# Performance work log

Hardware: AMD Instinct MI355X
Metric: run time of the kernel (lower is better)

## Reference

```python
import jax, jax.numpy as jnp
import numpy as np

N_OBSERVED = 64
N_LATENT = 64
N_NODES = N_OBSERVED + N_LATENT
M = 2                # max parents per node (BA attachment param)
N_SAMPLES = 262144
CAL_N = 256
CAL_FRAC = 0.1
SIGMA_W = 1.0


def _build_dag():
    """BA-style DAG in topological order: node i picks min(M, i) earlier parents."""
    rng = np.random.default_rng(0)
    par_idx = np.zeros((N_NODES, M), np.int32)
    par_mask = np.zeros((N_NODES, M), np.float32)
    is_root = np.zeros(N_NODES, bool)
    for i in range(N_NODES):
        k = min(M, i)
        if k == 0:
            is_root[i] = True
            continue
        ps = rng.choice(i, size=k, replace=False)
        par_idx[i, :k] = ps
        par_mask[i, :k] = 1.0
    has_child = np.zeros(N_NODES, bool)
    for i in range(N_NODES):
        for j in range(M):
            if par_mask[i, j] > 0:
                has_child[par_idx[i, j]] = True
    leaves = np.where(~has_child)[0]
    pool = leaves if len(leaves) >= N_OBSERVED else np.arange(N_NODES)
    chosen = rng.choice(pool, size=N_OBSERVED, replace=False).astype(np.int32)
    return par_idx, par_mask, is_root, chosen


def setup_inputs() -> dict:
    par_idx, par_mask, is_root, chosen = _build_dag()
    wrng = np.random.default_rng(1)
    n_par = par_mask.sum(axis=1)
    std = SIGMA_W / np.sqrt(np.maximum(n_par, 1.0))  # nn.init.normal_(std=sigma_w/sqrt(n_parents))
    W = (wrng.standard_normal((N_NODES, M)) * std[:, None] * par_mask).astype(np.float32)
    b = np.zeros(N_NODES, np.float32)                # bias zero-initialised
    key = jax.random.key(0)
    k1, k2, k3 = jax.random.split(key, 3)
    return {
        "n_samples": N_SAMPLES,
        "W": jnp.asarray(W),
        "b": jnp.asarray(b),
        "root_pilot": jax.random.normal(k1, (N_NODES, CAL_N), jnp.float32),
        "root_main": jax.random.normal(k2, (N_NODES, N_SAMPLES), jnp.float32),
        "z_noise": jax.random.normal(k3, (N_NODES, N_SAMPLES), jnp.float32),
        "par_mask": jnp.asarray(par_mask),
        "par_idx": jnp.asarray(par_idx),
        "is_root": jnp.asarray(is_root),
        "chosen": jnp.asarray(chosen),
    }


def _run_dag(W, b, par_mask, par_idx, is_root, roots, noise):
    """Topological scan: x_i = relu(w_i . x_parents + b_i) + noise_i, roots ~ given."""
    n = roots.shape[1]

    def step(vals, inp):
        i, pidx, pmask, w, bb, root_v, nz, rt = inp
        pv = vals[pidx]                                   # [M, n] gather parents
        h = jax.nn.relu(jnp.einsum("p,pn->n", w * pmask, pv) + bb) + nz
        v = jnp.where(rt, root_v, h)
        v = jnp.where(jnp.isfinite(v), v, jnp.zeros_like(v))
        vals = jax.lax.dynamic_update_slice(vals, v[None, :], (i, 0))
        return vals, None

    vals0 = jnp.zeros((N_NODES, n), roots.dtype)
    xs = (jnp.arange(N_NODES), par_idx, par_mask, W, b, roots, noise, is_root)
    vals, _ = jax.lax.scan(step, vals0, xs)
    return vals


def reference(n_samples, W, b, root_pilot, root_main, z_noise, par_mask, par_idx, is_root, chosen):
    # noise calibration: noiseless pilot pass, sigma_e = frac * IQR per node
    pilot = _run_dag(W, b, par_mask, par_idx, is_root, root_pilot, jnp.zeros_like(root_pilot))
    q75 = jnp.quantile(pilot, 0.75, axis=1)
    q25 = jnp.quantile(pilot, 0.25, axis=1)
    sigma_e = CAL_FRAC * jnp.maximum(q75 - q25, 1e-6)     # [N_NODES]
    # main pass with calibrated per-node noise
    vals = _run_dag(W, b, par_mask, par_idx, is_root, root_main, z_noise * sigma_e[:, None])
    return vals[chosen].T                                  # [n_samples, n_observed]
```

## Files before the change

kernel.cpp:

```cpp
#include <hip/hip_runtime.h>
#include <hip/hip_fp16.h>
#include <math.h>

#define NN   128
#define BS   64
#define SCAP 1056
#define RT_F 0x10000

#define IDX(n,t) ((n)*BS + ((t) ^ (((n)&15)<<1)))


__global__ __launch_bounds__(256) void prep_pilot_kernel(
    const float* __restrict__ W, const float* __restrict__ b,
    const float* __restrict__ pm, const int* __restrict__ pidx,
    const float* __restrict__ root_pilot,
    float4* __restrict__ wtab, int* __restrict__ pcode,
    int* __restrict__ slotmap, int* __restrict__ ngp,
    float* __restrict__ pilot_out, int CAL)
{
    __shared__ _Float16 vals[NN * 256];
    __shared__ int grp[NN], slot[NN], wcnt[4];
    __shared__ int nassigned, gdone, gfin;
    const int i = threadIdx.x, w = i >> 6, lane = i & 63;

    int p0 = 0, p1 = 0, rt = 1;
    float m0 = 0.f, m1 = 0.f;
    if (i < NN) {
        m0 = pm[2*i]; m1 = pm[2*i+1];
        p0 = pidx[2*i]; p1 = pidx[2*i+1];
        rt = (m0 == 0.0f && m1 == 0.0f) ? 1 : 0;
        grp[i] = -1; slot[i] = 0;
    }
    if (i == 0) { nassigned = 0; gdone = 0; gfin = 0; }
    __syncthreads();
    for (int g = 0; g < NN; ++g) {
        int ready = (i < NN) && (grp[i] < 0) && (rt || (grp[p0] >= 0 && grp[p1] >= 0));
        unsigned long long mask = __ballot(ready);
        if (lane == 0) wcnt[w] = __popcll(mask);
        __syncthreads();
        int base = 0;
        #pragma unroll
        for (int ww = 0; ww < 4; ++ww) if (ww < w) base += wcnt[ww];
        int r = base + __popcll(mask & ((1ull << lane) - 1ull));
        if (ready && r < 8) { grp[i] = g; slot[i] = g*8 + r; }
        if (i == 0) {
            int tot = wcnt[0] + wcnt[1] + wcnt[2] + wcnt[3];
            nassigned += min(tot, 8);
            if (nassigned >= NN) { gdone = 1; gfin = g; }
        }
        __syncthreads();
        if (gdone) break;
    }
    const int S0 = 8 * (gfin + 1);
    const int S  = (S0 + 31) & ~31;
    for (int k = i; k < SCAP; k += 256) {
        pcode[k] = RT_F;
        wtab[k]  = make_float4(0.f, 0.f, 0.f, 0.f);
    }
    __threadfence_block();
    __syncthreads();
    if (i < NN) {
        pcode[slot[i]] = p0 | (p1 << 8) | (rt << 16) | (i << 24);
        wtab[slot[i]]  = make_float4(W[2*i]*m0, W[2*i+1]*m1, b[i], 0.f);
        slotmap[i] = slot[i];
    }
    if (i == 0) ngp[0] = S;
    __threadfence_block();
    __syncthreads();

    const int jj = i;
    for (int s0 = 0; s0 < S; s0 += 8) {
        int pc[8]; float4 wv[8];
        #pragma unroll
        for (int u = 0; u < 8; ++u) pc[u] = pcode[s0 + u];
        #pragma unroll
        for (int u = 0; u < 8; ++u) wv[u] = wtab[s0 + u];
        float pa[8], pb[8];
        #pragma unroll
        for (int u = 0; u < 8; ++u) {
            int q0 = pc[u] & 0xff, q1 = (pc[u] >> 8) & 0xff;
            pa[u] = (float)vals[q0 * 256 + jj];
            pb[u] = (float)vals[q1 * 256 + jj];
        }
        _Float16 res[8]; int nodes[8]; float vf[8];
        #pragma unroll
        for (int u = 0; u < 8; ++u) {
            nodes[u] = (pc[u] >> 24) & 0xff;
            float v;
            if (pc[u] & RT_F) {
                v = root_pilot[nodes[u] * CAL + jj];
            } else {
                v = fmaxf(fmaf(wv[u].x, pa[u], fmaf(wv[u].y, pb[u], wv[u].z)), 0.0f);
            }
            if (!isfinite(v)) v = 0.0f;
            vf[u] = v; res[u] = (_Float16)v;
        }
        #pragma unroll
        for (int u = 0; u < 8; ++u) {
            vals[nodes[u] * 256 + jj] = res[u];
            pilot_out[nodes[u] * CAL + jj] = vf[u];
        }
    }
}

__global__ __launch_bounds__(256) void quant_kernel(
    const float* __restrict__ pilot, const int* __restrict__ slotmap,
    float4* __restrict__ wtab, int CAL)
{
    __shared__ float s[256];
    const int tid = threadIdx.x;
    const int node = blockIdx.x;
    s[tid] = pilot[(size_t)node * CAL + tid];
    __syncthreads();
    for (int k = 2; k <= 256; k <<= 1) {
        for (int jj = k >> 1; jj > 0; jj >>= 1) {
            int ixj = tid ^ jj;
            if (ixj > tid) {
                float a = s[tid], bv = s[ixj];
                bool up = ((tid & k) == 0);
                if ((a > bv) == up) { s[tid] = bv; s[ixj] = a; }
            }
            __syncthreads();
        }
    }
    if (tid == 0) {
        float q25 = s[63]  + 0.75f * (s[64]  - s[63]);
        float q75 = s[191] + 0.25f * (s[192] - s[191]);
        ((float*)&wtab[slotmap[node]])[3] = 0.1f * fmaxf(q75 - q25, 1e-6f);
    }
}

__device__ __forceinline__ void mk_chunk(
    int c, int P, float (&zb)[2][16],
    const int* __restrict__ pcode, const float4* __restrict__ wtab,
    const float* __restrict__ root_main, const float* __restrict__ z,
    unsigned NS, size_t j, _Float16* vals, int tid)
{
    const int base = c * 16;
    #pragma unroll
    for (int u = 0; u < 16; ++u) {
        int pcN = pcode[base + 16 + u];
        const float* src = (pcN & RT_F) ? root_main : z;
        unsigned node = (unsigned)(pcN >> 24) & 0xffu;
        zb[P ^ 1][u] = src[(size_t)(node * NS) + j];
    }
    #pragma unroll
    for (int h = 0; h < 2; ++h) {
        int pc[8];
        #pragma unroll
        for (int u = 0; u < 8; ++u) pc[u] = pcode[base + h*8 + u];
        float pa[8], pb[8];
        #pragma unroll
        for (int u = 0; u < 8; ++u) {
            int q0 = pc[u] & 0xff, q1 = (pc[u] >> 8) & 0xff;
            pa[u] = (float)vals[IDX(q0, tid)];
            pb[u] = (float)vals[IDX(q1, tid)];
        }
        _Float16 res[8]; int nodes[8];
        #pragma unroll
        for (int u = 0; u < 8; ++u) {
            float4 wv = wtab[base + h*8 + u];
            float zv = zb[P][h*8 + u];
            float v;
            if (pc[u] & RT_F) {
                v = zv;
            } else {
                v = fmaxf(fmaf(wv.x, pa[u], fmaf(wv.y, pb[u], wv.z)), 0.0f) + wv.w * zv;
            }
            if (!isfinite(v)) v = 0.0f;
            nodes[u] = (pc[u] >> 24) & 0xff;
            res[u] = (_Float16)v;
        }
        #pragma unroll
        for (int u = 0; u < 8; ++u) vals[IDX(nodes[u], tid)] = res[u];
    }
}

__global__ __launch_bounds__(64) void main_kernel(
    const float4* __restrict__ wtab, const int* __restrict__ pcode,
    const int* __restrict__ ngp,
    const float* __restrict__ root_main, const float* __restrict__ z,
    const int* __restrict__ chosen, float* __restrict__ out, int NSi)
{
    __shared__ _Float16 vals[NN * BS];
    const int tid = threadIdx.x;
    const size_t j = (size_t)blockIdx.x * BS + tid;
    const unsigned NS = (unsigned)NSi;
    const int S = ngp[0];
    const int nch = S >> 4;

    float zb[2][16];
    #pragma unroll
    for (int u = 0; u < 16; ++u) {
        int pc = pcode[u];
        const float* src = (pc & RT_F) ? root_main : z;
        unsigned node = (unsigned)(pc >> 24) & 0xffu;
        zb[0][u] = src[(size_t)(node * NS) + j];
    }

    for (int c = 0; c < nch; c += 2) {
        mk_chunk(c,     0, zb, pcode, wtab, root_main, z, NS, j, vals, tid);
        mk_chunk(c + 1, 1, zb, pcode, wtab, root_main, z, NS, j, vals, tid);
    }

    __syncthreads();

    float4* out4 = (float4*)(out + (size_t)blockIdx.x * BS * 64);
    #pragma unroll
    for (int it = 0; it < 16; ++it) {
        int cc = it * BS + tid;
        int s  = cc >> 4;
        int k0 = (cc & 15) << 2;
        int n0 = chosen[k0], n1 = chosen[k0+1], n2 = chosen[k0+2], n3 = chosen[k0+3];
        float4 o;
        o.x = (float)vals[IDX(n0, s)];
        o.y = (float)vals[IDX(n1, s)];
        o.z = (float)vals[IDX(n2, s)];
        o.w = (float)vals[IDX(n3, s)];
        out4[cc] = o;
    }
}

extern "C" void kernel_launch(void* const* d_in, const int* in_sizes, int n_in,
                              void* d_out, int out_size, void* d_ws, size_t ws_size,
                              hipStream_t stream) {
    const float* W          = (const float*)d_in[1];
    const float* b          = (const float*)d_in[2];
    const float* root_pilot = (const float*)d_in[3];
    const float* root_main  = (const float*)d_in[4];
    const float* z          = (const float*)d_in[5];
    const float* pm         = (const float*)d_in[6];
    const int*   pidx       = (const int*)d_in[7];
    const int*   chosen     = (const int*)d_in[9];
    float* out = (float*)d_out;

    const int NS  = in_sizes[4] / NN;
    const int CAL = in_sizes[3] / NN;

    char* ws = (char*)d_ws;
    float4* wtab    = (float4*)ws;
    int*    pcode   = (int*)(ws + 20480);
    int*    slotmap = (int*)(ws + 24704);
    int*    ngp     = (int*)(ws + 25216);
    float*  pilot   = (float*)(ws + 28672);

    prep_pilot_kernel<<<1, 256, 0, stream>>>(W, b, pm, pidx, root_pilot,
                                             wtab, pcode, slotmap, ngp, pilot, CAL);
    quant_kernel<<<NN, 256, 0, stream>>>(pilot, slotmap, wtab, CAL);
    main_kernel <<<NS / BS, BS, 0, stream>>>(wtab, pcode, ngp, root_main, z, chosen, out, NS);
}
```

Baseline: 337.9 us.

## Process two samples per thread with packed half2 shared storage and skip padding slots

Each thread in the main kernel now handles two adjacent samples, loading root/noise values as float2 and storing both results packed as a 32-bit half pair in shared memory with a new XOR swizzle. Padding slots in the schedule get a skip flag, so no global loads, shared reads or writes are issued for them in either the pilot or main kernel. This halves the grid size and the per-sample instruction overhead, at the cost of more registers per thread and fewer waves to hide memory latency.

```diff
diff --git a/kernel.cpp b/kernel.cpp
--- a/kernel.cpp
+++ b/kernel.cpp
@@ -2,12 +2,13 @@
 #include <hip/hip_fp16.h>
 #include <math.h>
 
-#define NN   128
-#define BS   64
-#define SCAP 1056
-#define RT_F 0x10000
-
-#define IDX(n,t) ((n)*BS + ((t) ^ (((n)&15)<<1)))
+#define NN    128
+#define SPB   128
+#define SCAP  1056
+#define RT_F  0x10000
+#define SK_F  0x20000
+
+#define WIDX(n,t) ((n)*64 + ((t) ^ ((n)&31)))
 
 
 __global__ __launch_bounds__(256) void prep_pilot_kernel(
@@ -54,7 +55,7 @@
     const int S0 = 8 * (gfin + 1);
     const int S  = (S0 + 31) & ~31;
     for (int k = i; k < SCAP; k += 256) {
-        pcode[k] = RT_F;
+        pcode[k] = RT_F | SK_F;
         wtab[k]  = make_float4(0.f, 0.f, 0.f, 0.f);
     }
     __threadfence_block();
@@ -78,27 +79,26 @@
         float pa[8], pb[8];
         #pragma unroll
         for (int u = 0; u < 8; ++u) {
-            int q0 = pc[u] & 0xff, q1 = (pc[u] >> 8) & 0xff;
-            pa[u] = (float)vals[q0 * 256 + jj];
-            pb[u] = (float)vals[q1 * 256 + jj];
-        }
-        _Float16 res[8]; int nodes[8]; float vf[8];
-        #pragma unroll
-        for (int u = 0; u < 8; ++u) {
-            nodes[u] = (pc[u] >> 24) & 0xff;
+            pa[u] = 0.f; pb[u] = 0.f;
+            if (!(pc[u] & (SK_F | RT_F))) {
+                int q0 = pc[u] & 0xff, q1 = (pc[u] >> 8) & 0xff;
+                pa[u] = (float)vals[q0 * 256 + jj];
+                pb[u] = (float)vals[q1 * 256 + jj];
+            }
+        }
+        #pragma unroll
+        for (int u = 0; u < 8; ++u) {
+            if (pc[u] & SK_F) continue;
+            int node = (pc[u] >> 24) & 0xff;
             float v;
             if (pc[u] & RT_F) {
-                v = root_pilot[nodes[u] * CAL + jj];
+                v = root_pilot[node * CAL + jj];
             } else {
                 v = fmaxf(fmaf(wv[u].x, pa[u], fmaf(wv[u].y, pb[u], wv[u].z)), 0.0f);
             }
             if (!isfinite(v)) v = 0.0f;
-            vf[u] = v; res[u] = (_Float16)v;
-        }
-        #pragma unroll
-        for (int u = 0; u < 8; ++u) {
-            vals[nodes[u] * 256 + jj] = res[u];
-            pilot_out[nodes[u] * CAL + jj] = vf[u];
+            vals[node * 256 + jj] = (_Float16)v;
+            pilot_out[node * CAL + jj] = v;
         }
     }
 }
@@ -131,48 +131,62 @@
 }
 
 __device__ __forceinline__ void mk_chunk(
-    int c, int P, float (&zb)[2][16],
+    int c, int P, float2 (&zb)[2][16],
     const int* __restrict__ pcode, const float4* __restrict__ wtab,
     const float* __restrict__ root_main, const float* __restrict__ z,
-    unsigned NS, size_t j, _Float16* vals, int tid)
+    unsigned NS, size_t j2, unsigned* vals, int tid)
 {
     const int base = c * 16;
     #pragma unroll
     for (int u = 0; u < 16; ++u) {
         int pcN = pcode[base + 16 + u];
-        const float* src = (pcN & RT_F) ? root_main : z;
-        unsigned node = (unsigned)(pcN >> 24) & 0xffu;
-        zb[P ^ 1][u] = src[(size_t)(node * NS) + j];
+        if (!(pcN & SK_F)) {
+            const float* src = (pcN & RT_F) ? root_main : z;
+            unsigned node = (unsigned)(pcN >> 24) & 0xffu;
+            zb[P ^ 1][u] = *(const float2*)(src + (size_t)node * NS + j2);
+        }
     }
     #pragma unroll
     for (int h = 0; h < 2; ++h) {
         int pc[8];
         #pragma unroll
         for (int u = 0; u < 8; ++u) pc[u] = pcode[base + h*8 + u];
-        float pa[8], pb[8];
-        #pragma unroll
-        for (int u = 0; u < 8; ++u) {
-            int q0 = pc[u] & 0xff, q1 = (pc[u] >> 8) & 0xff;
-            pa[u] = (float)vals[IDX(q0, tid)];
-            pb[u] = (float)vals[IDX(q1, tid)];
-        }
-        _Float16 res[8]; int nodes[8];
-        #pragma unroll
-        for (int u = 0; u < 8; ++u) {
+        unsigned wa[8], wb[8];
+        #pragma unroll
+        for (int u = 0; u < 8; ++u) {
+            wa[u] = 0u; wb[u] = 0u;
+            if (!(pc[u] & (SK_F | RT_F))) {
+                int q0 = pc[u] & 0xff, q1 = (pc[u] >> 8) & 0xff;
+                wa[u] = vals[WIDX(q0, tid)];
+                wb[u] = vals[WIDX(q1, tid)];
+            }
+        }
+        unsigned res[8]; int nodes[8];
+        #pragma unroll
+        for (int u = 0; u < 8; ++u) {
+            nodes[u] = (pc[u] >> 24) & 0xff;
             float4 wv = wtab[base + h*8 + u];
-            float zv = zb[P][h*8 + u];
-            float v;
+            float2 zv = zb[P][h*8 + u];
+            float v0, v1;
             if (pc[u] & RT_F) {
-                v = zv;
+                v0 = zv.x; v1 = zv.y;
             } else {
-                v = fmaxf(fmaf(wv.x, pa[u], fmaf(wv.y, pb[u], wv.z)), 0.0f) + wv.w * zv;
-            }
-            if (!isfinite(v)) v = 0.0f;
-            nodes[u] = (pc[u] >> 24) & 0xff;
-            res[u] = (_Float16)v;
-        }
-        #pragma unroll
-        for (int u = 0; u < 8; ++u) vals[IDX(nodes[u], tid)] = res[u];
+                union { unsigned u32; _Float16 h2[2]; } ua, ub;
+                ua.u32 = wa[u]; ub.u32 = wb[u];
+                float a0 = (float)ua.h2[0], a1 = (float)ua.h2[1];
+                float b0 = (float)ub.h2[0], b1 = (float)ub.h2[1];
+                v0 = fmaxf(fmaf(wv.x, a0, fmaf(wv.y, b0, wv.z)), 0.0f) + wv.w * zv.x;
+                v1 = fmaxf(fmaf(wv.x, a1, fmaf(wv.y, b1, wv.z)), 0.0f) + wv.w * zv.y;
+            }
+            if (!isfinite(v0)) v0 = 0.0f;
+            if (!isfinite(v1)) v1 = 0.0f;
+            union { unsigned u32; _Float16 h2[2]; } up;
+            up.h2[0] = (_Float16)v0; up.h2[1] = (_Float16)v1;
+            res[u] = up.u32;
+        }
+        #pragma unroll
+        for (int u = 0; u < 8; ++u)
+            if (!(pc[u] & SK_F)) vals[WIDX(nodes[u], tid)] = res[u];
     }
 }
 
@@ -182,41 +196,49 @@
     const float* __restrict__ root_main, const float* __restrict__ z,
     const int* __restrict__ chosen, float* __restrict__ out, int NSi)
 {
-    __shared__ _Float16 vals[NN * BS];
+    __shared__ unsigned vals[NN * 64];
     const int tid = threadIdx.x;
-    const size_t j = (size_t)blockIdx.x * BS + tid;
+    const size_t j2 = (size_t)blockIdx.x * SPB + (size_t)(tid * 2);
     const unsigned NS = (unsigned)NSi;
     const int S = ngp[0];
     const int nch = S >> 4;
 
-    float zb[2][16];
+    float2 zb[2][16];
     #pragma unroll
     for (int u = 0; u < 16; ++u) {
         int pc = pcode[u];
-        const float* src = (pc & RT_F) ? root_main : z;
-        unsigned node = (unsigned)(pc >> 24) & 0xffu;
-        zb[0][u] = src[(size_t)(node * NS) + j];
+        if (!(pc & SK_F)) {
+            const float* src = (pc & RT_F) ? root_main : z;
+            unsigned node = (unsigned)(pc >> 24) & 0xffu;
+            zb[0][u] = *(const float2*)(src + (size_t)node * NS + j2);
+        }
     }
 
     for (int c = 0; c < nch; c += 2) {
-        mk_chunk(c,     0, zb, pcode, wtab, root_main, z, NS, j, vals, tid);
-        mk_chunk(c + 1, 1, zb, pcode, wtab, root_main, z, NS, j, vals, tid);
-    }
-
-    __syncthreads();
-
-    float4* out4 = (float4*)(out + (size_t)blockIdx.x * BS * 64);
-    #pragma unroll
-    for (int it = 0; it < 16; ++it) {
-        int cc = it * BS + tid;
+        mk_chunk(c,     0, zb, pcode, wtab, root_main, z, NS, j2, vals, tid);
+        mk_chunk(c + 1, 1, zb, pcode, wtab, root_main, z, NS, j2, vals, tid);
+    }
+
+    __syncthreads();
+
+    float4* out4 = (float4*)(out + (size_t)blockIdx.x * SPB * 64);
+    #pragma unroll
+    for (int it = 0; it < 32; ++it) {
+        int cc = it * 64 + tid;
         int s  = cc >> 4;
         int k0 = (cc & 15) << 2;
         int n0 = chosen[k0], n1 = chosen[k0+1], n2 = chosen[k0+2], n3 = chosen[k0+3];
+        int tt = s >> 1, hh = s & 1;
+        union { unsigned u32; _Float16 h2[2]; } c0, c1, c2, c3;
+        c0.u32 = vals[WIDX(n0, tt)];
+        c1.u32 = vals[WIDX(n1, tt)];
+        c2.u32 = vals[WIDX(n2, tt)];
+        c3.u32 = vals[WIDX(n3, tt)];
         float4 o;
-        o.x = (float)vals[IDX(n0, s)];
-        o.y = (float)vals[IDX(n1, s)];
-        o.z = (float)vals[IDX(n2, s)];
-        o.w = (float)vals[IDX(n3, s)];
+        o.x = (float)c0.h2[hh];
+        o.y = (float)c1.h2[hh];
+        o.z = (float)c2.h2[hh];
+        o.w = (float)c3.h2[hh];
         out4[cc] = o;
     }
 }
@@ -247,5 +269,5 @@
     prep_pilot_kernel<<<1, 256, 0, stream>>>(W, b, pm, pidx, root_pilot,
                                              wtab, pcode, slotmap, ngp, pilot, CAL);
     quant_kernel<<<NN, 256, 0, stream>>>(pilot, slotmap, wtab, CAL);
-    main_kernel <<<NS / BS, BS, 0, stream>>>(wtab, pcode, ngp, root_main, z, chosen, out, NS);
-}
+    main_kernel <<<NS / SPB, 64, 0, stream>>>(wtab, pcode, ngp, root_main, z, chosen, out, NS);
+}
```

New measurement: 361.4 us. 1.07x slower.

## Deepen noise prefetch to four chunks and skip padding slots in DAG evaluation

Applied to the files above, without the earlier changes.

The main kernel now keeps four 16-slot chunks of root/noise loads in flight instead of a double buffer, which hides more global-memory latency behind the serial DAG computation. Padding slots get a skip flag, so they issue no global loads, no LDS reads and no stores. The slot count is rounded up to a multiple of 64 and the workspace offsets are widened to fit. The change raises register pressure (64 prefetch floats per thread) and adds per-slot branches.

```diff
diff --git a/kernel.cpp b/kernel.cpp
--- a/kernel.cpp
+++ b/kernel.cpp
@@ -2,10 +2,11 @@
 #include <hip/hip_fp16.h>
 #include <math.h>
 
-#define NN   128
-#define BS   64
-#define SCAP 1056
-#define RT_F 0x10000
+#define NN    128
+#define BS    64
+#define SCAP  1280
+#define RT_F  0x10000
+#define SK_F  0x20000
 
 #define IDX(n,t) ((n)*BS + ((t) ^ (((n)&15)<<1)))
 
@@ -52,9 +53,9 @@
         if (gdone) break;
     }
     const int S0 = 8 * (gfin + 1);
-    const int S  = (S0 + 31) & ~31;
+    const int S  = (S0 + 63) & ~63;
     for (int k = i; k < SCAP; k += 256) {
-        pcode[k] = RT_F;
+        pcode[k] = RT_F | SK_F;
         wtab[k]  = make_float4(0.f, 0.f, 0.f, 0.f);
     }
     __threadfence_block();
@@ -78,27 +79,26 @@
         float pa[8], pb[8];
         #pragma unroll
         for (int u = 0; u < 8; ++u) {
-            int q0 = pc[u] & 0xff, q1 = (pc[u] >> 8) & 0xff;
-            pa[u] = (float)vals[q0 * 256 + jj];
-            pb[u] = (float)vals[q1 * 256 + jj];
-        }
-        _Float16 res[8]; int nodes[8]; float vf[8];
-        #pragma unroll
-        for (int u = 0; u < 8; ++u) {
-            nodes[u] = (pc[u] >> 24) & 0xff;
+            pa[u] = 0.f; pb[u] = 0.f;
+            if (!(pc[u] & (SK_F | RT_F))) {
+                int q0 = pc[u] & 0xff, q1 = (pc[u] >> 8) & 0xff;
+                pa[u] = (float)vals[q0 * 256 + jj];
+                pb[u] = (float)vals[q1 * 256 + jj];
+            }
+        }
+        #pragma unroll
+        for (int u = 0; u < 8; ++u) {
+            if (pc[u] & SK_F) continue;
+            int node = (pc[u] >> 24) & 0xff;
             float v;
             if (pc[u] & RT_F) {
-                v = root_pilot[nodes[u] * CAL + jj];
+                v = root_pilot[node * CAL + jj];
             } else {
                 v = fmaxf(fmaf(wv[u].x, pa[u], fmaf(wv[u].y, pb[u], wv[u].z)), 0.0f);
             }
             if (!isfinite(v)) v = 0.0f;
-            vf[u] = v; res[u] = (_Float16)v;
-        }
-        #pragma unroll
-        for (int u = 0; u < 8; ++u) {
-            vals[nodes[u] * 256 + jj] = res[u];
-            pilot_out[nodes[u] * CAL + jj] = vf[u];
+            vals[node * 256 + jj] = (_Float16)v;
+            pilot_out[node * CAL + jj] = v;
         }
     }
 }
@@ -130,20 +130,30 @@
     }
 }
 
-__device__ __forceinline__ void mk_chunk(
-    int c, int P, float (&zb)[2][16],
-    const int* __restrict__ pcode, const float4* __restrict__ wtab,
+__device__ __forceinline__ void pf_chunk(
+    float (&zb)[16], int c,
+    const int* __restrict__ pcode,
     const float* __restrict__ root_main, const float* __restrict__ z,
-    unsigned NS, size_t j, _Float16* vals, int tid)
+    unsigned NS, size_t j)
 {
     const int base = c * 16;
     #pragma unroll
     for (int u = 0; u < 16; ++u) {
-        int pcN = pcode[base + 16 + u];
-        const float* src = (pcN & RT_F) ? root_main : z;
-        unsigned node = (unsigned)(pcN >> 24) & 0xffu;
-        zb[P ^ 1][u] = src[(size_t)(node * NS) + j];
-    }
+        int pc = pcode[base + u];
+        if (!(pc & SK_F)) {
+            const float* src = (pc & RT_F) ? root_main : z;
+            unsigned node = (unsigned)(pc >> 24) & 0xffu;
+            zb[u] = src[(size_t)(node * NS) + j];
+        }
+    }
+}
+
+__device__ __forceinline__ void comp_chunk(
+    float (&zb)[16], int c,
+    const int* __restrict__ pcode, const float4* __restrict__ wtab,
+    _Float16* vals, int tid)
+{
+    const int base = c * 16;
     #pragma unroll
     for (int h = 0; h < 2; ++h) {
         int pc[8];
@@ -152,15 +162,19 @@
         float pa[8], pb[8];
         #pragma unroll
         for (int u = 0; u < 8; ++u) {
-            int q0 = pc[u] & 0xff, q1 = (pc[u] >> 8) & 0xff;
-            pa[u] = (float)vals[IDX(q0, tid)];
-            pb[u] = (float)vals[IDX(q1, tid)];
+            pa[u] = 0.f; pb[u] = 0.f;
+            if (!(pc[u] & (SK_F | RT_F))) {
+                int q0 = pc[u] & 0xff, q1 = (pc[u] >> 8) & 0xff;
+                pa[u] = (float)vals[IDX(q0, tid)];
+                pb[u] = (float)vals[IDX(q1, tid)];
+            }
         }
         _Float16 res[8]; int nodes[8];
         #pragma unroll
         for (int u = 0; u < 8; ++u) {
+            nodes[u] = (pc[u] >> 24) & 0xff;
             float4 wv = wtab[base + h*8 + u];
-            float zv = zb[P][h*8 + u];
+            float zv = zb[h*8 + u];
             float v;
             if (pc[u] & RT_F) {
                 v = zv;
@@ -168,11 +182,11 @@
                 v = fmaxf(fmaf(wv.x, pa[u], fmaf(wv.y, pb[u], wv.z)), 0.0f) + wv.w * zv;
             }
             if (!isfinite(v)) v = 0.0f;
-            nodes[u] = (pc[u] >> 24) & 0xff;
             res[u] = (_Float16)v;
         }
         #pragma unroll
-        for (int u = 0; u < 8; ++u) vals[IDX(nodes[u], tid)] = res[u];
+        for (int u = 0; u < 8; ++u)
+            if (!(pc[u] & SK_F)) vals[IDX(nodes[u], tid)] = res[u];
     }
 }
 
@@ -189,18 +203,21 @@
     const int S = ngp[0];
     const int nch = S >> 4;
 
-    float zb[2][16];
-    #pragma unroll
-    for (int u = 0; u < 16; ++u) {
-        int pc = pcode[u];
-        const float* src = (pc & RT_F) ? root_main : z;
-        unsigned node = (unsigned)(pc >> 24) & 0xffu;
-        zb[0][u] = src[(size_t)(node * NS) + j];
-    }
-
-    for (int c = 0; c < nch; c += 2) {
-        mk_chunk(c,     0, zb, pcode, wtab, root_main, z, NS, j, vals, tid);
-        mk_chunk(c + 1, 1, zb, pcode, wtab, root_main, z, NS, j, vals, tid);
+    float zA[16], zB[16], zC[16], zD[16];
+    pf_chunk(zA, 0, pcode, root_main, z, NS, j);
+    pf_chunk(zB, 1, pcode, root_main, z, NS, j);
+    pf_chunk(zC, 2, pcode, root_main, z, NS, j);
+    pf_chunk(zD, 3, pcode, root_main, z, NS, j);
+
+    for (int c = 0; c < nch; c += 4) {
+        comp_chunk(zA, c,   pcode, wtab, vals, tid);
+        pf_chunk  (zA, c+4, pcode, root_main, z, NS, j);
+        comp_chunk(zB, c+1, pcode, wtab, vals, tid);
+        pf_chunk  (zB, c+5, pcode, root_main, z, NS, j);
+        comp_chunk(zC, c+2, pcode, wtab, vals, tid);
+        pf_chunk  (zC, c+6, pcode, root_main, z, NS, j);
+        comp_chunk(zD, c+3, pcode, wtab, vals, tid);
+        pf_chunk  (zD, c+7, pcode, root_main, z, NS, j);
     }
 
     __syncthreads();
@@ -240,8 +257,8 @@
     char* ws = (char*)d_ws;
     float4* wtab    = (float4*)ws;
     int*    pcode   = (int*)(ws + 20480);
-    int*    slotmap = (int*)(ws + 24704);
-    int*    ngp     = (int*)(ws + 25216);
+    int*    slotmap = (int*)(ws + 25600);
+    int*    ngp     = (int*)(ws + 26112);
     float*  pilot   = (float*)(ws + 28672);
 
     prep_pilot_kernel<<<1, 256, 0, stream>>>(W, b, pm, pidx, root_pilot,
```

After: 359.7 us. 1.06x slower.
